# Optimization experiments

Measured on AMD Instinct MI355X. Metric: run time of the kernel, lower is better.

The kernel has to match this reference:

```python
import jax, jax.numpy as jnp
import numpy as np

NUM_HEADS = 12
HEAD_DIM = 64
HIDDEN = NUM_HEADS * HEAD_DIM  # 768


def setup_inputs() -> dict:
    key = jax.random.key(0)
    ks = jax.random.split(key, 18)
    B, Ni, Nt, H = 8, 1024, 512, HIDDEN
    inp = {
        "hidden_states": jax.random.normal(ks[0], (B, Ni, H), jnp.float32),
        "text": jax.random.normal(ks[1], (B, Nt, H), jnp.float32),
    }
    names = ["Wq", "Wk", "Wv", "Wqt", "Wkt", "Wvt", "Wo"]
    for i, n in enumerate(names):
        inp[n] = jax.random.normal(ks[2 + i], (H, H), jnp.float32) * 0.02
        inp["b" + n[1:]] = jnp.zeros((H,), jnp.float32)
    return inp


def _split_heads(x):
    # [B, S, H] -> [B, h, S, dh]
    B, S, _ = x.shape
    return x.reshape(B, S, NUM_HEADS, HEAD_DIM).transpose(0, 2, 1, 3)


def _merge_heads(x):
    # [B, h, S, dh] -> [B, S, H]
    B, h, S, dh = x.shape
    return x.transpose(0, 2, 1, 3).reshape(B, S, h * dh)


def _attend(q, k, v):
    scale = 1.0 / jnp.sqrt(jnp.asarray(HEAD_DIM, q.dtype))
    scores = jnp.einsum("bhqd,bhkd->bhqk", q, k) * scale
    probs = jax.nn.softmax(scores, axis=-1)
    ctx = jnp.einsum("bhqk,bhkd->bhqd", probs, v)
    return ctx, probs


def reference(hidden_states, text, Wq, bq, Wk, bk, Wv, bv,
              Wqt, bqt, Wkt, bkt, Wvt, bvt, Wo, bo):
    q_i = _split_heads(hidden_states @ Wq + bq)
    k_i = _split_heads(hidden_states @ Wk + bk)
    v_i = _split_heads(hidden_states @ Wv + bv)
    q_t = _split_heads(text @ Wqt + bqt)
    k_t = _split_heads(text @ Wkt + bkt)
    v_t = _split_heads(text @ Wvt + bvt)

    ctx_ii, weights = _attend(q_i, k_i, v_i)   # img -> img (weights returned, vis=True)
    ctx_tt, _ = _attend(q_t, k_t, v_t)         # text -> text
    ctx_it, _ = _attend(q_i, k_t, v_t)         # img queries, text keys/values
    ctx_ti, _ = _attend(q_t, k_i, v_i)         # text queries, img keys/values

    out_img = (_merge_heads(ctx_ii) + _merge_heads(ctx_it)) * 0.5 @ Wo + bo
    out_text = (_merge_heads(ctx_tt) + _merge_heads(ctx_ti)) * 0.5 @ Wo + bo
    return out_img, out_text, weights
```

## Files before the change

### kernel.cpp

```cpp
#include <hip/hip_runtime.h>

typedef __attribute__((ext_vector_type(4))) float f32x4;
typedef __attribute__((ext_vector_type(8))) short short8;
typedef __attribute__((ext_vector_type(4))) unsigned short us4;
typedef unsigned short u16;

__device__ __forceinline__ u16 f2b(float f) {
  union { float f; unsigned u; } a; a.f = f;
  unsigned r = a.u + 0x7fffu + ((a.u >> 16) & 1u);
  return (u16)(r >> 16);
}
#define SWZ(r, byteoff) ((((r) * 128) + (byteoff)) ^ (((r) & 7) << 4))

typedef __attribute__((address_space(1))) const void* gp1;
typedef __attribute__((address_space(3))) void* lp3;
__device__ __forceinline__ void gload16(const void* g, void* lds_wave_uniform_base) {
  __builtin_amdgcn_global_load_lds((gp1)g, (lp3)lds_wave_uniform_base, 16, 0, 0);
}

__global__ __launch_bounds__(256) void wtrans_kernel(
    const float* w0, const float* w1, const float* w2, const float* w3,
    const float* w4, const float* w5, const float* w6, u16* wt)
{
  const float* Ws[7] = {w0, w1, w2, w3, w4, w5, w6};
  const float* W = Ws[blockIdx.z];
  u16* out = wt + (size_t)blockIdx.z * 768 * 768;
  __shared__ float tile[64][65];
  const int t = threadIdx.x;
  const int r0 = blockIdx.y * 64, c0 = blockIdx.x * 64;
#pragma unroll
  for (int i = 0; i < 4; ++i) {
    int idx = i * 256 + t;
    int r = idx >> 4, c = (idx & 15) * 4;
    f32x4 v = *(const f32x4*)(W + (size_t)(r0 + r) * 768 + (c0 + c));
    tile[r][c + 0] = v[0]; tile[r][c + 1] = v[1];
    tile[r][c + 2] = v[2]; tile[r][c + 3] = v[3];
  }
  __syncthreads();
#pragma unroll
  for (int i = 0; i < 4; ++i) {
    int idx = i * 256 + t;
    int rn = idx >> 4, c = (idx & 15) * 4;
    us4 o;
    o[0] = f2b(tile[c + 0][rn]); o[1] = f2b(tile[c + 1][rn]);
    o[2] = f2b(tile[c + 2][rn]); o[3] = f2b(tile[c + 3][rn]);
    *(us4*)(out + (size_t)(c0 + rn) * 768 + (r0 + c)) = o;
  }
}

__global__ __launch_bounds__(256) void xconv_kernel(
    const float* __restrict__ h, const float* __restrict__ tx, u16* __restrict__ o)
{
  size_t e = ((size_t)blockIdx.x * 256 + threadIdx.x) * 8;
  const float* src; size_t off;
  if (e < 6291456) { src = h; off = e; } else { src = tx; off = e - 6291456; }
  f32x4 v0 = *(const f32x4*)(src + off), v1 = *(const f32x4*)(src + off + 4);
  short8 r;
  r[0] = (short)f2b(v0[0]); r[1] = (short)f2b(v0[1]); r[2] = (short)f2b(v0[2]); r[3] = (short)f2b(v0[3]);
  r[4] = (short)f2b(v1[0]); r[5] = (short)f2b(v1[1]); r[6] = (short)f2b(v1[2]); r[7] = (short)f2b(v1[3]);
  *(short8*)(o + e) = r;
}

__global__ __launch_bounds__(256) void proj_kernel(
    const u16* __restrict__ Xb, const u16* __restrict__ Wt3,
    const float* __restrict__ ba, const float* __restrict__ bb, const float* __restrict__ bc,
    u16* __restrict__ oa, u16* __restrict__ ob, u16* __restrict__ oc,
    int S, int logS)
{
  const int m0 = blockIdx.x * 128;
  const int y = blockIdx.y;
  const int z = y / 6;
  const int n0 = (y % 6) * 128;
  const u16* Wt = Wt3 + (size_t)y * 128 * 768;
  const float* bias = (z == 0) ? ba : (z == 1) ? bb : bc;
  u16* out = (z == 0) ? oa : (z == 1) ? ob : oc;
  const bool vmode = (z == 2);
  __shared__ unsigned char sm[36864];
  unsigned char* Asm = sm;
  unsigned char* Bsm = sm + 16384;
  const int t = threadIdx.x, w = t >> 6, l = t & 63;
  const int wm = (w & 1) * 64, wn = (w >> 1) * 64;
  f32x4 acc[4][4] = {};
  for (int k0 = 0; k0 < 768; k0 += 64) {
#pragma unroll
    for (int j = 0; j < 4; ++j) {
      int chunk = j * 4 + w;
      int r = chunk * 8 + (l >> 3);
      int cb = ((l & 7) * 16) ^ ((r & 7) << 4);
      gload16(Xb + (size_t)(m0 + r) * 768 + k0 + cb / 2, Asm + chunk * 1024);
    }
#pragma unroll
    for (int j = 0; j < 4; ++j) {
      int chunk = j * 4 + w;
      int r = chunk * 8 + (l >> 3);
      int cb = ((l & 7) * 16) ^ ((r & 7) << 4);
      gload16(Wt + (size_t)r * 768 + k0 + cb / 2, Bsm + chunk * 1024);
    }
    __syncthreads();
#pragma unroll
    for (int kc = 0; kc < 2; ++kc) {
      short8 af[4], bfr[4];
      const int koff = (kc * 32 + (l >> 4) * 8) * 2;
#pragma unroll
      for (int ms = 0; ms < 4; ++ms) {
        int row = wm + ms * 16 + (l & 15);
        af[ms] = *(const short8*)(Asm + SWZ(row, koff));
      }
#pragma unroll
      for (int ns = 0; ns < 4; ++ns) {
        int row = wn + ns * 16 + (l & 15);
        bfr[ns] = *(const short8*)(Bsm + SWZ(row, koff));
      }
#pragma unroll
      for (int ms = 0; ms < 4; ++ms)
#pragma unroll
        for (int ns = 0; ns < 4; ++ns)
          acc[ms][ns] = __builtin_amdgcn_mfma_f32_16x16x32_bf16(af[ms], bfr[ns], acc[ms][ns], 0, 0, 0);
    }
    __syncthreads();
  }
  float bv[4];
#pragma unroll
  for (int ns = 0; ns < 4; ++ns) bv[ns] = bias[n0 + wn + ns * 16 + (l & 15)];
#pragma unroll
  for (int ms = 0; ms < 4; ++ms)
#pragma unroll
    for (int ns = 0; ns < 4; ++ns)
#pragma unroll
      for (int i = 0; i < 4; ++i) {
        u16 u = f2b(acc[ms][ns][i] + bv[ns]);
        int mm = wm + ms * 16 + (l >> 4) * 4 + i;
        int nn = wn + ns * 16 + (l & 15);
        int row = vmode ? nn : mm, col = vmode ? mm : nn;
        *(u16*)(sm + row * 272 + col * 2) = u;
      }
  __syncthreads();
  if (!vmode) {
#pragma unroll
    for (int i = 0; i < 8; ++i) {
      int idx = i * 256 + t;
      int r = idx >> 4, c = (idx & 15) * 8;
      short8 v = *(const short8*)(sm + r * 272 + c * 2);
      int sg = m0 + r, b = sg >> logS, s = sg & (S - 1);
      int n = n0 + c, hh = n >> 6, d = n & 63;
      *(short8*)(out + (((size_t)b * 12 + hh) * S + s) * 64 + d) = v;
    }
  } else {
#pragma unroll
    for (int i = 0; i < 8; ++i) {
      int idx = i * 256 + t;
      int r = idx >> 4, c = (idx & 15) * 8;
      short8 v = *(const short8*)(sm + r * 272 + c * 2);
      int n = n0 + r, hh = n >> 6, d = n & 63;
      int sg = m0 + c, b = sg >> logS, s = sg & (S - 1);
      *(short8*)(out + (((size_t)b * 12 + hh) * 64 + d) * S + s) = v;
    }
  }
}

__device__ __forceinline__ void stage_k(const u16* Kp, int kt, unsigned char* Ksm, int w, int l) {
#pragma unroll
  for (int j = 0; j < 2; ++j) {
    int chunk = j * 4 + w;
    int r = chunk * 8 + (l >> 3);
    int cb = ((l & 7) * 16) ^ ((r & 7) << 4);
    gload16(Kp + (size_t)(kt * 64 + r) * 64 + cb / 2, Ksm + chunk * 1024);
  }
}
__device__ __forceinline__ void stage_v(const u16* Vp, int kt, int Sk, unsigned char* Vsm, int w, int l) {
#pragma unroll
  for (int j = 0; j < 2; ++j) {
    int chunk = j * 4 + w;
    int r = chunk * 8 + (l >> 3);
    int cb = ((l & 7) * 16) ^ ((r & 7) << 4);
    gload16(Vp + (size_t)r * Sk + kt * 64 + cb / 2, Vsm + chunk * 1024);
  }
}
__device__ __forceinline__ void qk_mfma(const short8 qf[2], const unsigned char* Ksm, int l, f32x4 sfr[4]) {
#pragma unroll
  for (int kc = 0; kc < 2; ++kc)
#pragma unroll
    for (int sub = 0; sub < 4; ++sub) {
      int row = sub * 16 + (l & 15);
      short8 kf = *(const short8*)(Ksm + SWZ(row, (kc * 32 + (l >> 4) * 8) * 2));
      sfr[sub] = __builtin_amdgcn_mfma_f32_16x16x32_bf16(qf[kc], kf, sfr[sub], 0, 0, 0);
    }
}
__device__ __forceinline__ void red16(float v[4]) {
#pragma unroll
  for (int d = 1; d < 16; d <<= 1)
#pragma unroll
    for (int i = 0; i < 4; ++i) v[i] += __shfl_xor(v[i], d);
}
__device__ __forceinline__ void attn_unnorm_pass(
    const u16* Kp, const u16* Vp, int Sk, const short8 qf[2],
    unsigned char* Ksm, unsigned char* Vsm, unsigned char* Psm,
    int w, int l, f32x4 og[4], float ll[4])
{
  const int nkt = Sk >> 6;
  for (int kt = 0; kt < nkt; ++kt) {
    stage_k(Kp, kt, Ksm, w, l);
    stage_v(Vp, kt, Sk, Vsm, w, l);
    __syncthreads();
    f32x4 sfr[4] = {};
    qk_mfma(qf, Ksm, l, sfr);
#pragma unroll
    for (int sub = 0; sub < 4; ++sub)
#pragma unroll
      for (int i = 0; i < 4; ++i) {
        float p = __expf(sfr[sub][i] * 0.125f);
        ll[i] += p;
        *(u16*)(Psm + SWZ((l >> 4) * 4 + i, (sub * 16 + (l & 15)) * 2)) = f2b(p);
      }
    short8 pa[2];
    pa[0] = *(const short8*)(Psm + SWZ(l & 15, ((l >> 4) * 8) * 2));
    pa[1] = *(const short8*)(Psm + SWZ(l & 15, (32 + (l >> 4) * 8) * 2));
#pragma unroll
    for (int kc = 0; kc < 2; ++kc)
#pragma unroll
      for (int ds = 0; ds < 4; ++ds) {
        int row = ds * 16 + (l & 15);
        short8 vb = *(const short8*)(Vsm + SWZ(row, (kc * 32 + (l >> 4) * 8) * 2));
        og[ds] = __builtin_amdgcn_mfma_f32_16x16x32_bf16(pa[kc], vb, og[ds], 0, 0, 0);
      }
    __syncthreads();
  }
}

__global__ __launch_bounds__(256) void attn2_kernel(
    const u16* __restrict__ Q,
    const u16* __restrict__ KA, const u16* __restrict__ VA, int SkA,
    const u16* __restrict__ KB, const u16* __restrict__ VB, int SkB,
    u16* __restrict__ CTX, float* __restrict__ PROBS, int Sq)
{
  const int h = blockIdx.y, b = blockIdx.z;
  const int q0 = blockIdx.x * 64;
  const int t = threadIdx.x, w = t >> 6, l = t & 63;
  const size_t bh = (size_t)b * 12 + h;
  const u16* Qp = Q + bh * (size_t)Sq * 64;
  const u16* KpA = KA + bh * (size_t)SkA * 64;
  const u16* VpA = VA + bh * (size_t)64 * SkA;
  const u16* KpB = KB + bh * (size_t)SkB * 64;
  const u16* VpB = VB + bh * (size_t)64 * SkB;
  __shared__ unsigned char smem[41984];
  unsigned char* Ksm = smem;
  unsigned char* Vsm = smem + 8192;
  unsigned char* Psm = smem + 16384 + w * 2048;
  unsigned char* Pf  = smem + 24576 + w * 4352;

  short8 qf[2];
  {
    int row = q0 + w * 16 + (l & 15);
    qf[0] = *(const short8*)(Qp + (size_t)row * 64 + (l >> 4) * 8);
    qf[1] = *(const short8*)(Qp + (size_t)row * 64 + 32 + (l >> 4) * 8);
  }

  f32x4 of[4] = {};
  if (PROBS) {
    float ll[4] = {0.f, 0.f, 0.f, 0.f};
    const int nkt = SkA >> 6;
    for (int kt = 0; kt < nkt; ++kt) {
      stage_k(KpA, kt, Ksm, w, l);
      __syncthreads();
      f32x4 sfr[4] = {};
      qk_mfma(qf, Ksm, l, sfr);
#pragma unroll
      for (int sub = 0; sub < 4; ++sub)
#pragma unroll
        for (int i = 0; i < 4; ++i) ll[i] += __expf(sfr[sub][i] * 0.125f);
      __syncthreads();
    }
    red16(ll);
    float rl[4];
#pragma unroll
    for (int i = 0; i < 4; ++i) rl[i] = 1.0f / ll[i];
    const size_t pbase = (bh * Sq + q0 + w * 16);
    for (int kt = 0; kt < nkt; ++kt) {
      stage_k(KpA, kt, Ksm, w, l);
      stage_v(VpA, kt, SkA, Vsm, w, l);
      __syncthreads();
      f32x4 sfr[4] = {};
      qk_mfma(qf, Ksm, l, sfr);
#pragma unroll
      for (int sub = 0; sub < 4; ++sub)
#pragma unroll
        for (int i = 0; i < 4; ++i) {
          float p = __expf(sfr[sub][i] * 0.125f) * rl[i];
          int prow = (l >> 4) * 4 + i, pcol = sub * 16 + (l & 15);
          *(float*)(Pf + prow * 272 + pcol * 4) = p;
          *(u16*)(Psm + SWZ(prow, pcol * 2)) = f2b(p);
        }
#pragma unroll
      for (int ps = 0; ps < 4; ++ps) {
        int row = ps * 4 + (l >> 4);
        f32x4 v = *(const f32x4*)(Pf + row * 272 + (l & 15) * 16);
        *(f32x4*)(PROBS + (pbase + row) * (size_t)SkA + kt * 64 + (l & 15) * 4) = v;
      }
      short8 pa[2];
      pa[0] = *(const short8*)(Psm + SWZ(l & 15, ((l >> 4) * 8) * 2));
      pa[1] = *(const short8*)(Psm + SWZ(l & 15, (32 + (l >> 4) * 8) * 2));
#pragma unroll
      for (int kc = 0; kc < 2; ++kc)
#pragma unroll
        for (int ds = 0; ds < 4; ++ds) {
          int row = ds * 16 + (l & 15);
          short8 vb = *(const short8*)(Vsm + SWZ(row, (kc * 32 + (l >> 4) * 8) * 2));
          of[ds] = __builtin_amdgcn_mfma_f32_16x16x32_bf16(pa[kc], vb, of[ds], 0, 0, 0);
        }
      __syncthreads();
    }
#pragma unroll
    for (int ds = 0; ds < 4; ++ds) of[ds] *= 0.5f;
  } else {
    float ll[4] = {0.f, 0.f, 0.f, 0.f};
    attn_unnorm_pass(KpA, VpA, SkA, qf, Ksm, Vsm, Psm, w, l, of, ll);
    red16(ll);
#pragma unroll
    for (int ds = 0; ds < 4; ++ds)
#pragma unroll
      for (int i = 0; i < 4; ++i) of[ds][i] *= 0.5f / ll[i];
  }
  {
    f32x4 og[4] = {};
    float l2[4] = {0.f, 0.f, 0.f, 0.f};
    attn_unnorm_pass(KpB, VpB, SkB, qf, Ksm, Vsm, Psm, w, l, og, l2);
    red16(l2);
#pragma unroll
    for (int ds = 0; ds < 4; ++ds)
#pragma unroll
      for (int i = 0; i < 4; ++i) of[ds][i] += og[ds][i] * (0.5f / l2[i]);
  }
#pragma unroll
  for (int ds = 0; ds < 4; ++ds)
#pragma unroll
    for (int i = 0; i < 4; ++i) {
      int prow = (l >> 4) * 4 + i, pcol = ds * 16 + (l & 15);
      *(u16*)(Psm + SWZ(prow, pcol * 2)) = f2b(of[ds][i]);
    }
#pragma unroll
  for (int i = 0; i < 2; ++i) {
    int idx = i * 64 + l;
    int r = idx >> 3, off = (idx & 7) * 16;
    short8 v = *(const short8*)(Psm + SWZ(r, off));
    int s = q0 + w * 16 + r;
    *(short8*)(CTX + ((size_t)b * Sq + s) * 768 + h * 64 + off / 2) = v;
  }
}

__global__ __launch_bounds__(256) void outproj_kernel(
    const u16* __restrict__ C, const u16* __restrict__ Wt,
    const float* __restrict__ bias, float* __restrict__ OUT)
{
  const int m0 = blockIdx.x * 128, n0 = blockIdx.y * 128;
  __shared__ unsigned char sm[32768];
  unsigned char* Asm = sm;
  unsigned char* Bsm = sm + 16384;
  const int t = threadIdx.x, w = t >> 6, l = t & 63;
  const int wm = (w & 1) * 64, wn = (w >> 1) * 64;
  f32x4 acc[4][4] = {};
  for (int k0 = 0; k0 < 768; k0 += 64) {
#pragma unroll
    for (int j = 0; j < 4; ++j) {
      int chunk = j * 4 + w;
      int r = chunk * 8 + (l >> 3);
      int cb = ((l & 7) * 16) ^ ((r & 7) << 4);
      gload16(C + (size_t)(m0 + r) * 768 + k0 + cb / 2, Asm + chunk * 1024);
    }
#pragma unroll
    for (int j = 0; j < 4; ++j) {
      int chunk = j * 4 + w;
      int r = chunk * 8 + (l >> 3);
      int cb = ((l & 7) * 16) ^ ((r & 7) << 4);
      gload16(Wt + (size_t)(n0 + r) * 768 + k0 + cb / 2, Bsm + chunk * 1024);
    }
    __syncthreads();
#pragma unroll
    for (int kc = 0; kc < 2; ++kc) {
      short8 af[4], bfr[4];
      const int koff = (kc * 32 + (l >> 4) * 8) * 2;
#pragma unroll
      for (int ms = 0; ms < 4; ++ms) {
        int row = wm + ms * 16 + (l & 15);
        af[ms] = *(const short8*)(Asm + SWZ(row, koff));
      }
#pragma unroll
      for (int ns = 0; ns < 4; ++ns) {
        int row = wn + ns * 16 + (l & 15);
        bfr[ns] = *(const short8*)(Bsm + SWZ(row, koff));
      }
#pragma unroll
      for (int ms = 0; ms < 4; ++ms)
#pragma unroll
        for (int ns = 0; ns < 4; ++ns)
          acc[ms][ns] = __builtin_amdgcn_mfma_f32_16x16x32_bf16(af[ms], bfr[ns], acc[ms][ns], 0, 0, 0);
    }
    __syncthreads();
  }
#pragma unroll
  for (int ms = 0; ms < 4; ++ms)
#pragma unroll
    for (int ns = 0; ns < 4; ++ns) {
      float bv = bias[n0 + wn + ns * 16 + (l & 15)];
#pragma unroll
      for (int i = 0; i < 4; ++i) {
        int mm = m0 + wm + ms * 16 + (l >> 4) * 4 + i;
        int nn = n0 + wn + ns * 16 + (l & 15);
        OUT[(size_t)mm * 768 + nn] = acc[ms][ns][i] + bv;
      }
    }
}

extern "C" void kernel_launch(void* const* d_in, const int* in_sizes, int n_in,
                              void* d_out, int out_size, void* d_ws, size_t ws_size,
                              hipStream_t stream)
{
  const float* hidden = (const float*)d_in[0];
  const float* text   = (const float*)d_in[1];
  const float* Wq  = (const float*)d_in[2];  const float* bq  = (const float*)d_in[3];
  const float* Wk  = (const float*)d_in[4];  const float* bk  = (const float*)d_in[5];
  const float* Wv  = (const float*)d_in[6];  const float* bv  = (const float*)d_in[7];
  const float* Wqt = (const float*)d_in[8];  const float* bqt = (const float*)d_in[9];
  const float* Wkt = (const float*)d_in[10]; const float* bkt = (const float*)d_in[11];
  const float* Wvt = (const float*)d_in[12]; const float* bvt = (const float*)d_in[13];
  const float* Wo  = (const float*)d_in[14]; const float* bo  = (const float*)d_in[15];

  u16* wt   = (u16*)d_ws;
  u16* xb   = wt + 7 * 589824;
  u16* qi   = xb + 9437184;
  u16* ki   = qi + 6291456;
  u16* vti  = ki + 6291456;
  u16* qt   = vti + 6291456;
  u16* ktx  = qt + 3145728;
  u16* vtt  = ktx + 3145728;
  u16* cimg = vtt + 3145728;
  u16* ctxt = cimg + 6291456;

  float* out_img  = (float*)d_out;
  float* out_text = out_img + 6291456;
  float* weights  = out_text + 3145728;

  wtrans_kernel<<<dim3(12, 12, 7), 256, 0, stream>>>(Wq, Wk, Wv, Wqt, Wkt, Wvt, Wo, wt);
  xconv_kernel<<<4608, 256, 0, stream>>>(hidden, text, xb);

  u16* wto = wt + 6 * 589824;
  proj_kernel<<<dim3(64, 18), 256, 0, stream>>>(xb, wt, bq, bk, bv, qi, ki, vti, 1024, 10);
  proj_kernel<<<dim3(32, 18), 256, 0, stream>>>(xb + 6291456, wt + 3 * 589824,
                                                bqt, bkt, bvt, qt, ktx, vtt, 512, 9);

  attn2_kernel<<<dim3(16, 12, 8), 256, 0, stream>>>(qi, ki, vti, 1024, ktx, vtt, 512,
                                                    cimg, weights, 1024);
  attn2_kernel<<<dim3(8, 12, 8), 256, 0, stream>>>(qt, ktx, vtt, 512, ki, vti, 1024,
                                                   ctxt, nullptr, 512);

  outproj_kernel<<<dim3(64, 6), 256, 0, stream>>>(cimg, wto, bo, out_img);
  outproj_kernel<<<dim3(32, 6), 256, 0, stream>>>(ctxt, wto, bo, out_text);
}
```

Baseline: 363.4 us.

## Merge launches, double-buffer K/V in attention, add MFMA priority hints

Merges the weight-transpose and input-conversion kernels into one launch, and merges the image and text variants of the projection, attention and output-projection kernels into single launches. Each merged kernel uses a remapped block index so work is spread across the XCDs. The attention kernel double-buffers the K/V tiles in LDS so the next tile loads while the current one is computed, which removes one barrier per iteration. It also keeps probabilities in fp32 LDS and converts them to bf16 right before the PV MFMA. s_setprio hints are wrapped around the MFMA loops, and LDS use per attention block grows, which may lower occupancy.

```diff
diff --git a/kernel.cpp b/kernel.cpp
--- a/kernel.cpp
+++ b/kernel.cpp
@@ -4,6 +4,7 @@
 typedef __attribute__((ext_vector_type(8))) short short8;
 typedef __attribute__((ext_vector_type(4))) unsigned short us4;
 typedef unsigned short u16;
+typedef unsigned char uchar;
 
 __device__ __forceinline__ u16 f2b(float f) {
   union { float f; unsigned u; } a; a.f = f;
@@ -18,62 +19,70 @@
   __builtin_amdgcn_global_load_lds((gp1)g, (lp3)lds_wave_uniform_base, 16, 0, 0);
 }
 
-__global__ __launch_bounds__(256) void wtrans_kernel(
+__global__ __launch_bounds__(256) void prep_kernel(
     const float* w0, const float* w1, const float* w2, const float* w3,
-    const float* w4, const float* w5, const float* w6, u16* wt)
+    const float* w4, const float* w5, const float* w6, u16* wt,
+    const float* __restrict__ h, const float* __restrict__ tx, u16* __restrict__ xb)
 {
-  const float* Ws[7] = {w0, w1, w2, w3, w4, w5, w6};
-  const float* W = Ws[blockIdx.z];
-  u16* out = wt + (size_t)blockIdx.z * 768 * 768;
-  __shared__ float tile[64][65];
-  const int t = threadIdx.x;
-  const int r0 = blockIdx.y * 64, c0 = blockIdx.x * 64;
-#pragma unroll
-  for (int i = 0; i < 4; ++i) {
-    int idx = i * 256 + t;
-    int r = idx >> 4, c = (idx & 15) * 4;
-    f32x4 v = *(const f32x4*)(W + (size_t)(r0 + r) * 768 + (c0 + c));
-    tile[r][c + 0] = v[0]; tile[r][c + 1] = v[1];
-    tile[r][c + 2] = v[2]; tile[r][c + 3] = v[3];
-  }
-  __syncthreads();
-#pragma unroll
-  for (int i = 0; i < 4; ++i) {
-    int idx = i * 256 + t;
-    int rn = idx >> 4, c = (idx & 15) * 4;
-    us4 o;
-    o[0] = f2b(tile[c + 0][rn]); o[1] = f2b(tile[c + 1][rn]);
-    o[2] = f2b(tile[c + 2][rn]); o[3] = f2b(tile[c + 3][rn]);
-    *(us4*)(out + (size_t)(c0 + rn) * 768 + (r0 + c)) = o;
-  }
-}
-
-__global__ __launch_bounds__(256) void xconv_kernel(
-    const float* __restrict__ h, const float* __restrict__ tx, u16* __restrict__ o)
+  const int bid = blockIdx.x, t = threadIdx.x;
+  if (bid < 1008) {
+    __shared__ float tile[64][65];
+    const float* Ws[7] = {w0, w1, w2, w3, w4, w5, w6};
+    int z = bid / 144, rem = bid % 144;
+    const float* W = Ws[z];
+    u16* out = wt + (size_t)z * 589824;
+    const int r0 = (rem / 12) * 64, c0 = (rem % 12) * 64;
+#pragma unroll
+    for (int i = 0; i < 4; ++i) {
+      int idx = i * 256 + t;
+      int r = idx >> 4, c = (idx & 15) * 4;
+      f32x4 v = *(const f32x4*)(W + (size_t)(r0 + r) * 768 + (c0 + c));
+      tile[r][c + 0] = v[0]; tile[r][c + 1] = v[1];
+      tile[r][c + 2] = v[2]; tile[r][c + 3] = v[3];
+    }
+    __syncthreads();
+#pragma unroll
+    for (int i = 0; i < 4; ++i) {
+      int idx = i * 256 + t;
+      int rn = idx >> 4, c = (idx & 15) * 4;
+      us4 o;
+      o[0] = f2b(tile[c + 0][rn]); o[1] = f2b(tile[c + 1][rn]);
+      o[2] = f2b(tile[c + 2][rn]); o[3] = f2b(tile[c + 3][rn]);
+      *(us4*)(out + (size_t)(c0 + rn) * 768 + (r0 + c)) = o;
+    }
+  } else {
+    size_t e = ((size_t)(bid - 1008) * 256 + t) * 8;
+    const float* src; size_t off;
+    if (e < 6291456) { src = h; off = e; } else { src = tx; off = e - 6291456; }
+    f32x4 v0 = *(const f32x4*)(src + off), v1 = *(const f32x4*)(src + off + 4);
+    short8 r;
+    r[0] = (short)f2b(v0[0]); r[1] = (short)f2b(v0[1]); r[2] = (short)f2b(v0[2]); r[3] = (short)f2b(v0[3]);
+    r[4] = (short)f2b(v1[0]); r[5] = (short)f2b(v1[1]); r[6] = (short)f2b(v1[2]); r[7] = (short)f2b(v1[3]);
+    *(short8*)(xb + e) = r;
+  }
+}
+
+__global__ __launch_bounds__(256) void proj_kernel(
+    const u16* __restrict__ Xb, const u16* __restrict__ wt,
+    const float* __restrict__ bq, const float* __restrict__ bk, const float* __restrict__ bv,
+    const float* __restrict__ bqt, const float* __restrict__ bkt, const float* __restrict__ bvt,
+    u16* __restrict__ qi, u16* __restrict__ ki, u16* __restrict__ vti,
+    u16* __restrict__ qt, u16* __restrict__ ktx, u16* __restrict__ vtt)
 {
-  size_t e = ((size_t)blockIdx.x * 256 + threadIdx.x) * 8;
-  const float* src; size_t off;
-  if (e < 6291456) { src = h; off = e; } else { src = tx; off = e - 6291456; }
-  f32x4 v0 = *(const f32x4*)(src + off), v1 = *(const f32x4*)(src + off + 4);
-  short8 r;
-  r[0] = (short)f2b(v0[0]); r[1] = (short)f2b(v0[1]); r[2] = (short)f2b(v0[2]); r[3] = (short)f2b(v0[3]);
-  r[4] = (short)f2b(v1[0]); r[5] = (short)f2b(v1[1]); r[6] = (short)f2b(v1[2]); r[7] = (short)f2b(v1[3]);
-  *(short8*)(o + e) = r;
-}
-
-__global__ __launch_bounds__(256) void proj_kernel(
-    const u16* __restrict__ Xb, const u16* __restrict__ Wt3,
-    const float* __restrict__ ba, const float* __restrict__ bb, const float* __restrict__ bc,
-    u16* __restrict__ oa, u16* __restrict__ ob, u16* __restrict__ oc,
-    int S, int logS)
-{
-  const int m0 = blockIdx.x * 128;
-  const int y = blockIdx.y;
-  const int z = y / 6;
-  const int n0 = (y % 6) * 128;
-  const u16* Wt = Wt3 + (size_t)y * 128 * 768;
-  const float* bias = (z == 0) ? ba : (z == 1) ? bb : bc;
-  u16* out = (z == 0) ? oa : (z == 1) ? ob : oc;
+  const int bid = blockIdx.x;
+  const int wk = (bid & 7) * 216 + (bid >> 3);
+  const bool img = wk < 1152;
+  const int id = img ? wk : wk - 1152;
+  const int y = img ? (id >> 6) : (id >> 5);
+  const int x = img ? (id & 63) : (id & 31);
+  const int z = y / 6, n0 = (y % 6) * 128, m0 = x * 128;
+  const int S = img ? 1024 : 512, logS = img ? 10 : 9;
+  const u16* X = img ? Xb : Xb + 6291456;
+  const u16* Wt = wt + (img ? 0 : (size_t)3 * 589824) + (size_t)y * 98304;
+  const float* bias = img ? (z == 0 ? bq : z == 1 ? bk : bv)
+                          : (z == 0 ? bqt : z == 1 ? bkt : bvt);
+  u16* out = img ? (z == 0 ? qi : z == 1 ? ki : vti)
+                 : (z == 0 ? qt : z == 1 ? ktx : vtt);
   const bool vmode = (z == 2);
   __shared__ unsigned char sm[36864];
   unsigned char* Asm = sm;
@@ -87,7 +96,7 @@
       int chunk = j * 4 + w;
       int r = chunk * 8 + (l >> 3);
       int cb = ((l & 7) * 16) ^ ((r & 7) << 4);
-      gload16(Xb + (size_t)(m0 + r) * 768 + k0 + cb / 2, Asm + chunk * 1024);
+      gload16(X + (size_t)(m0 + r) * 768 + k0 + cb / 2, Asm + chunk * 1024);
     }
 #pragma unroll
     for (int j = 0; j < 4; ++j) {
@@ -111,24 +120,26 @@
         int row = wn + ns * 16 + (l & 15);
         bfr[ns] = *(const short8*)(Bsm + SWZ(row, koff));
       }
+      __builtin_amdgcn_s_setprio(1);
 #pragma unroll
       for (int ms = 0; ms < 4; ++ms)
 #pragma unroll
         for (int ns = 0; ns < 4; ++ns)
           acc[ms][ns] = __builtin_amdgcn_mfma_f32_16x16x32_bf16(af[ms], bfr[ns], acc[ms][ns], 0, 0, 0);
-    }
-    __syncthreads();
-  }
-  float bv[4];
-#pragma unroll
-  for (int ns = 0; ns < 4; ++ns) bv[ns] = bias[n0 + wn + ns * 16 + (l & 15)];
+      __builtin_amdgcn_s_setprio(0);
+    }
+    __syncthreads();
+  }
+  float bvv[4];
+#pragma unroll
+  for (int ns = 0; ns < 4; ++ns) bvv[ns] = bias[n0 + wn + ns * 16 + (l & 15)];
 #pragma unroll
   for (int ms = 0; ms < 4; ++ms)
 #pragma unroll
     for (int ns = 0; ns < 4; ++ns)
 #pragma unroll
       for (int i = 0; i < 4; ++i) {
-        u16 u = f2b(acc[ms][ns][i] + bv[ns]);
+        u16 u = f2b(acc[ms][ns][i] + bvv[ns]);
         int mm = wm + ms * 16 + (l >> 4) * 4 + i;
         int nn = wn + ns * 16 + (l & 15);
         int row = vmode ? nn : mm, col = vmode ? mm : nn;
@@ -158,7 +169,7 @@
   }
 }
 
-__device__ __forceinline__ void stage_k(const u16* Kp, int kt, unsigned char* Ksm, int w, int l) {
+__device__ __forceinline__ void stage_k(const u16* Kp, int kt, uchar* Ksm, int w, int l) {
 #pragma unroll
   for (int j = 0; j < 2; ++j) {
     int chunk = j * 4 + w;
@@ -167,7 +178,7 @@
     gload16(Kp + (size_t)(kt * 64 + r) * 64 + cb / 2, Ksm + chunk * 1024);
   }
 }
-__device__ __forceinline__ void stage_v(const u16* Vp, int kt, int Sk, unsigned char* Vsm, int w, int l) {
+__device__ __forceinline__ void stage_v(const u16* Vp, int kt, int Sk, uchar* Vsm, int w, int l) {
 #pragma unroll
   for (int j = 0; j < 2; ++j) {
     int chunk = j * 4 + w;
@@ -176,7 +187,8 @@
     gload16(Vp + (size_t)r * Sk + kt * 64 + cb / 2, Vsm + chunk * 1024);
   }
 }
-__device__ __forceinline__ void qk_mfma(const short8 qf[2], const unsigned char* Ksm, int l, f32x4 sfr[4]) {
+__device__ __forceinline__ void qk8(const short8 qf[2], const uchar* Ksm, int l, f32x4 sfr[4]) {
+  __builtin_amdgcn_s_setprio(1);
 #pragma unroll
   for (int kc = 0; kc < 2; ++kc)
 #pragma unroll
@@ -185,6 +197,29 @@
       short8 kf = *(const short8*)(Ksm + SWZ(row, (kc * 32 + (l >> 4) * 8) * 2));
       sfr[sub] = __builtin_amdgcn_mfma_f32_16x16x32_bf16(qf[kc], kf, sfr[sub], 0, 0, 0);
     }
+  __builtin_amdgcn_s_setprio(0);
+}
+__device__ __forceinline__ void pv8(const uchar* Pf, const uchar* Vsm, int l, f32x4 og[4]) {
+  const uchar* base = Pf + (l & 15) * 272 + (l >> 4) * 32;
+  f32x4 a0 = *(const f32x4*)(base);
+  f32x4 a1 = *(const f32x4*)(base + 16);
+  f32x4 b0 = *(const f32x4*)(base + 128);
+  f32x4 b1 = *(const f32x4*)(base + 144);
+  short8 pa0, pa1;
+  pa0[0] = (short)f2b(a0[0]); pa0[1] = (short)f2b(a0[1]); pa0[2] = (short)f2b(a0[2]); pa0[3] = (short)f2b(a0[3]);
+  pa0[4] = (short)f2b(a1[0]); pa0[5] = (short)f2b(a1[1]); pa0[6] = (short)f2b(a1[2]); pa0[7] = (short)f2b(a1[3]);
+  pa1[0] = (short)f2b(b0[0]); pa1[1] = (short)f2b(b0[1]); pa1[2] = (short)f2b(b0[2]); pa1[3] = (short)f2b(b0[3]);
+  pa1[4] = (short)f2b(b1[0]); pa1[5] = (short)f2b(b1[1]); pa1[6] = (short)f2b(b1[2]); pa1[7] = (short)f2b(b1[3]);
+  __builtin_amdgcn_s_setprio(1);
+#pragma unroll
+  for (int ds = 0; ds < 4; ++ds) {
+    int row = ds * 16 + (l & 15);
+    short8 vb0 = *(const short8*)(Vsm + SWZ(row, ((l >> 4) * 8) * 2));
+    short8 vb1 = *(const short8*)(Vsm + SWZ(row, (32 + (l >> 4) * 8) * 2));
+    og[ds] = __builtin_amdgcn_mfma_f32_16x16x32_bf16(pa0, vb0, og[ds], 0, 0, 0);
+    og[ds] = __builtin_amdgcn_mfma_f32_16x16x32_bf16(pa1, vb1, og[ds], 0, 0, 0);
+  }
+  __builtin_amdgcn_s_setprio(0);
 }
 __device__ __forceinline__ void red16(float v[4]) {
 #pragma unroll
@@ -192,61 +227,67 @@
 #pragma unroll
     for (int i = 0; i < 4; ++i) v[i] += __shfl_xor(v[i], d);
 }
-__device__ __forceinline__ void attn_unnorm_pass(
+__device__ __forceinline__ void pass_unnorm(
     const u16* Kp, const u16* Vp, int Sk, const short8 qf[2],
-    unsigned char* Ksm, unsigned char* Vsm, unsigned char* Psm,
+    uchar* Ks0, uchar* Ks1, uchar* Vs0, uchar* Vs1, uchar* Pf,
     int w, int l, f32x4 og[4], float ll[4])
 {
   const int nkt = Sk >> 6;
+  stage_k(Kp, 0, Ks0, w, l);
+  stage_v(Vp, 0, Sk, Vs0, w, l);
+  __syncthreads();
   for (int kt = 0; kt < nkt; ++kt) {
-    stage_k(Kp, kt, Ksm, w, l);
-    stage_v(Vp, kt, Sk, Vsm, w, l);
-    __syncthreads();
+    uchar* Kc = (kt & 1) ? Ks1 : Ks0;
+    uchar* Vc = (kt & 1) ? Vs1 : Vs0;
+    if (kt + 1 < nkt) {
+      stage_k(Kp, kt + 1, (kt & 1) ? Ks0 : Ks1, w, l);
+      stage_v(Vp, kt + 1, Sk, (kt & 1) ? Vs0 : Vs1, w, l);
+    }
     f32x4 sfr[4] = {};
-    qk_mfma(qf, Ksm, l, sfr);
+    qk8(qf, Kc, l, sfr);
 #pragma unroll
     for (int sub = 0; sub < 4; ++sub)
 #pragma unroll
       for (int i = 0; i < 4; ++i) {
         float p = __expf(sfr[sub][i] * 0.125f);
         ll[i] += p;
-        *(u16*)(Psm + SWZ((l >> 4) * 4 + i, (sub * 16 + (l & 15)) * 2)) = f2b(p);
-      }
-    short8 pa[2];
-    pa[0] = *(const short8*)(Psm + SWZ(l & 15, ((l >> 4) * 8) * 2));
-    pa[1] = *(const short8*)(Psm + SWZ(l & 15, (32 + (l >> 4) * 8) * 2));
-#pragma unroll
-    for (int kc = 0; kc < 2; ++kc)
-#pragma unroll
-      for (int ds = 0; ds < 4; ++ds) {
-        int row = ds * 16 + (l & 15);
-        short8 vb = *(const short8*)(Vsm + SWZ(row, (kc * 32 + (l >> 4) * 8) * 2));
-        og[ds] = __builtin_amdgcn_mfma_f32_16x16x32_bf16(pa[kc], vb, og[ds], 0, 0, 0);
-      }
-    __syncthreads();
-  }
-}
-
-__global__ __launch_bounds__(256) void attn2_kernel(
-    const u16* __restrict__ Q,
-    const u16* __restrict__ KA, const u16* __restrict__ VA, int SkA,
-    const u16* __restrict__ KB, const u16* __restrict__ VB, int SkB,
-    u16* __restrict__ CTX, float* __restrict__ PROBS, int Sq)
+        *(float*)(Pf + ((l >> 4) * 4 + i) * 272 + (sub * 16 + (l & 15)) * 4) = p;
+      }
+    pv8(Pf, Vc, l, og);
+    __syncthreads();
+  }
+}
+
+__global__ __launch_bounds__(256) void attn_kernel(
+    const u16* __restrict__ qi, const u16* __restrict__ ki, const u16* __restrict__ vti,
+    const u16* __restrict__ qt, const u16* __restrict__ ktx, const u16* __restrict__ vtt,
+    u16* __restrict__ cimg, u16* __restrict__ ctxt, float* __restrict__ weights)
 {
-  const int h = blockIdx.y, b = blockIdx.z;
-  const int q0 = blockIdx.x * 64;
+  __shared__ uchar smem[50176];
   const int t = threadIdx.x, w = t >> 6, l = t & 63;
-  const size_t bh = (size_t)b * 12 + h;
-  const u16* Qp = Q + bh * (size_t)Sq * 64;
-  const u16* KpA = KA + bh * (size_t)SkA * 64;
-  const u16* VpA = VA + bh * (size_t)64 * SkA;
-  const u16* KpB = KB + bh * (size_t)SkB * 64;
-  const u16* VpB = VB + bh * (size_t)64 * SkB;
-  __shared__ unsigned char smem[41984];
-  unsigned char* Ksm = smem;
-  unsigned char* Vsm = smem + 8192;
-  unsigned char* Psm = smem + 16384 + w * 2048;
-  unsigned char* Pf  = smem + 24576 + w * 4352;
+  uchar* Ks0 = smem;
+  uchar* Ks1 = smem + 8192;
+  uchar* Vs0 = smem + 16384;
+  uchar* Vs1 = smem + 24576;
+  uchar* Pf  = smem + 32768 + w * 4352;
+
+  const int bid = blockIdx.x;
+  const int wk = (bid & 7) * 288 + (bid >> 3);
+  const bool img = wk < 1536;
+  const int id = img ? wk : wk - 1536;
+  const int x = img ? (id & 15) : (id & 7);
+  const int head = img ? (id >> 4) : (id >> 3);
+  const int b = head / 12, h = head % 12;
+  const int Sq = img ? 1024 : 512;
+  const int SkA = img ? 1024 : 512, SkB = img ? 512 : 1024;
+  const u16* Qp = (img ? qi : qt) + (size_t)head * Sq * 64;
+  const u16* KpA = (img ? ki : ktx) + (size_t)head * SkA * 64;
+  const u16* VpA = (img ? vti : vtt) + (size_t)head * 64 * SkA;
+  const u16* KpB = (img ? ktx : ki) + (size_t)head * SkB * 64;
+  const u16* VpB = (img ? vtt : vti) + (size_t)head * 64 * SkB;
+  u16* CTX = img ? cimg : ctxt;
+  float* PROBS = img ? weights : nullptr;
+  const int q0 = x * 64;
 
   short8 qf[2];
   {
@@ -259,36 +300,42 @@
   if (PROBS) {
     float ll[4] = {0.f, 0.f, 0.f, 0.f};
     const int nkt = SkA >> 6;
+    stage_k(KpA, 0, Ks0, w, l);
+    __syncthreads();
     for (int kt = 0; kt < nkt; ++kt) {
-      stage_k(KpA, kt, Ksm, w, l);
-      __syncthreads();
+      uchar* Kc = (kt & 1) ? Ks1 : Ks0;
+      if (kt + 1 < nkt) stage_k(KpA, kt + 1, (kt & 1) ? Ks0 : Ks1, w, l);
       f32x4 sfr[4] = {};
-      qk_mfma(qf, Ksm, l, sfr);
+      qk8(qf, Kc, l, sfr);
 #pragma unroll
       for (int sub = 0; sub < 4; ++sub)
 #pragma unroll
         for (int i = 0; i < 4; ++i) ll[i] += __expf(sfr[sub][i] * 0.125f);
       __syncthreads();
     }
+    stage_k(KpA, 0, Ks0, w, l);
+    stage_v(VpA, 0, SkA, Vs0, w, l);
     red16(ll);
     float rl[4];
 #pragma unroll
     for (int i = 0; i < 4; ++i) rl[i] = 1.0f / ll[i];
-    const size_t pbase = (bh * Sq + q0 + w * 16);
+    __syncthreads();
+    const size_t pbase = ((size_t)head * Sq + q0 + w * 16);
     for (int kt = 0; kt < nkt; ++kt) {
-      stage_k(KpA, kt, Ksm, w, l);
-      stage_v(VpA, kt, SkA, Vsm, w, l);
-      __syncthreads();
+      uchar* Kc = (kt & 1) ? Ks1 : Ks0;
+      uchar* Vc = (kt & 1) ? Vs1 : Vs0;
+      if (kt + 1 < nkt) {
+        stage_k(KpA, kt + 1, (kt & 1) ? Ks0 : Ks1, w, l);
+        stage_v(VpA, kt + 1, SkA, (kt & 1) ? Vs0 : Vs1, w, l);
+      }
       f32x4 sfr[4] = {};
-      qk_mfma(qf, Ksm, l, sfr);
+      qk8(qf, Kc, l, sfr);
 #pragma unroll
       for (int sub = 0; sub < 4; ++sub)
 #pragma unroll
         for (int i = 0; i < 4; ++i) {
           float p = __expf(sfr[sub][i] * 0.125f) * rl[i];
-          int prow = (l >> 4) * 4 + i, pcol = sub * 16 + (l & 15);
-          *(float*)(Pf + prow * 272 + pcol * 4) = p;
-          *(u16*)(Psm + SWZ(prow, pcol * 2)) = f2b(p);
+          *(float*)(Pf + ((l >> 4) * 4 + i) * 272 + (sub * 16 + (l & 15)) * 4) = p;
         }
 #pragma unroll
       for (int ps = 0; ps < 4; ++ps) {
@@ -296,24 +343,14 @@
         f32x4 v = *(const f32x4*)(Pf + row * 272 + (l & 15) * 16);
         *(f32x4*)(PROBS + (pbase + row) * (size_t)SkA + kt * 64 + (l & 15) * 4) = v;
       }
-      short8 pa[2];
-      pa[0] = *(const short8*)(Psm + SWZ(l & 15, ((l >> 4) * 8) * 2));
-      pa[1] = *(const short8*)(Psm + SWZ(l & 15, (32 + (l >> 4) * 8) * 2));
-#pragma unroll
-      for (int kc = 0; kc < 2; ++kc)
-#pragma unroll
-        for (int ds = 0; ds < 4; ++ds) {
-          int row = ds * 16 + (l & 15);
-          short8 vb = *(const short8*)(Vsm + SWZ(row, (kc * 32 + (l >> 4) * 8) * 2));
-          of[ds] = __builtin_amdgcn_mfma_f32_16x16x32_bf16(pa[kc], vb, of[ds], 0, 0, 0);
-        }
+      pv8(Pf, Vc, l, of);
       __syncthreads();
     }
 #pragma unroll
     for (int ds = 0; ds < 4; ++ds) of[ds] *= 0.5f;
   } else {
     float ll[4] = {0.f, 0.f, 0.f, 0.f};
-    attn_unnorm_pass(KpA, VpA, SkA, qf, Ksm, Vsm, Psm, w, l, of, ll);
+    pass_unnorm(KpA, VpA, SkA, qf, Ks0, Ks1, Vs0, Vs1, Pf, w, l, of, ll);
     red16(ll);
 #pragma unroll
     for (int ds = 0; ds < 4; ++ds)
@@ -323,7 +360,7 @@
   {
     f32x4 og[4] = {};
     float l2[4] = {0.f, 0.f, 0.f, 0.f};
-    attn_unnorm_pass(KpB, VpB, SkB, qf, Ksm, Vsm, Psm, w, l, og, l2);
+    pass_unnorm(KpB, VpB, SkB, qf, Ks0, Ks1, Vs0, Vs1, Pf, w, l, og, l2);
     red16(l2);
 #pragma unroll
     for (int ds = 0; ds < 4; ++ds)
@@ -333,25 +370,36 @@
 #pragma unroll
   for (int ds = 0; ds < 4; ++ds)
 #pragma unroll
-    for (int i = 0; i < 4; ++i) {
-      int prow = (l >> 4) * 4 + i, pcol = ds * 16 + (l & 15);
-      *(u16*)(Psm + SWZ(prow, pcol * 2)) = f2b(of[ds][i]);
-    }
+    for (int i = 0; i < 4; ++i)
+      *(float*)(Pf + ((l >> 4) * 4 + i) * 272 + (ds * 16 + (l & 15)) * 4) = of[ds][i];
 #pragma unroll
   for (int i = 0; i < 2; ++i) {
-    int idx = i * 64 + l;
-    int r = idx >> 3, off = (idx & 7) * 16;
-    short8 v = *(const short8*)(Psm + SWZ(r, off));
+    int it = i * 64 + l;
+    int r = it >> 3, cg = it & 7;
+    f32x4 v0 = *(const f32x4*)(Pf + r * 272 + cg * 32);
+    f32x4 v1 = *(const f32x4*)(Pf + r * 272 + cg * 32 + 16);
+    short8 o;
+    o[0] = (short)f2b(v0[0]); o[1] = (short)f2b(v0[1]); o[2] = (short)f2b(v0[2]); o[3] = (short)f2b(v0[3]);
+    o[4] = (short)f2b(v1[0]); o[5] = (short)f2b(v1[1]); o[6] = (short)f2b(v1[2]); o[7] = (short)f2b(v1[3]);
     int s = q0 + w * 16 + r;
-    *(short8*)(CTX + ((size_t)b * Sq + s) * 768 + h * 64 + off / 2) = v;
+    *(short8*)(CTX + ((size_t)b * Sq + s) * 768 + h * 64 + cg * 8) = o;
   }
 }
 
 __global__ __launch_bounds__(256) void outproj_kernel(
-    const u16* __restrict__ C, const u16* __restrict__ Wt,
-    const float* __restrict__ bias, float* __restrict__ OUT)
+    const u16* __restrict__ cimg, const u16* __restrict__ ctxt,
+    const u16* __restrict__ Wto, const float* __restrict__ bias,
+    float* __restrict__ out_img, float* __restrict__ out_text)
 {
-  const int m0 = blockIdx.x * 128, n0 = blockIdx.y * 128;
+  const int bid = blockIdx.x;
+  const int wk = (bid & 7) * 72 + (bid >> 3);
+  const bool img = wk < 384;
+  const int id = img ? wk : wk - 384;
+  const int y = img ? (id >> 6) : (id >> 5);
+  const int x = img ? (id & 63) : (id & 31);
+  const u16* C = img ? cimg : ctxt;
+  float* OUT = img ? out_img : out_text;
+  const int m0 = x * 128, n0 = y * 128;
   __shared__ unsigned char sm[32768];
   unsigned char* Asm = sm;
   unsigned char* Bsm = sm + 16384;
@@ -371,7 +419,7 @@
       int chunk = j * 4 + w;
       int r = chunk * 8 + (l >> 3);
       int cb = ((l & 7) * 16) ^ ((r & 7) << 4);
-      gload16(Wt + (size_t)(n0 + r) * 768 + k0 + cb / 2, Bsm + chunk * 1024);
+      gload16(Wto + (size_t)(n0 + r) * 768 + k0 + cb / 2, Bsm + chunk * 1024);
     }
     __syncthreads();
 #pragma unroll
@@ -388,11 +436,13 @@
         int row = wn + ns * 16 + (l & 15);
         bfr[ns] = *(const short8*)(Bsm + SWZ(row, koff));
       }
+      __builtin_amdgcn_s_setprio(1);
 #pragma unroll
       for (int ms = 0; ms < 4; ++ms)
 #pragma unroll
         for (int ns = 0; ns < 4; ++ns)
           acc[ms][ns] = __builtin_amdgcn_mfma_f32_16x16x32_bf16(af[ms], bfr[ns], acc[ms][ns], 0, 0, 0);
+      __builtin_amdgcn_s_setprio(0);
     }
     __syncthreads();
   }
@@ -439,19 +489,12 @@
   float* out_text = out_img + 6291456;
   float* weights  = out_text + 3145728;
 
-  wtrans_kernel<<<dim3(12, 12, 7), 256, 0, stream>>>(Wq, Wk, Wv, Wqt, Wkt, Wvt, Wo, wt);
-  xconv_kernel<<<4608, 256, 0, stream>>>(hidden, text, xb);
-
-  u16* wto = wt + 6 * 589824;
-  proj_kernel<<<dim3(64, 18), 256, 0, stream>>>(xb, wt, bq, bk, bv, qi, ki, vti, 1024, 10);
-  proj_kernel<<<dim3(32, 18), 256, 0, stream>>>(xb + 6291456, wt + 3 * 589824,
-                                                bqt, bkt, bvt, qt, ktx, vtt, 512, 9);
-
-  attn2_kernel<<<dim3(16, 12, 8), 256, 0, stream>>>(qi, ki, vti, 1024, ktx, vtt, 512,
-                                                    cimg, weights, 1024);
-  attn2_kernel<<<dim3(8, 12, 8), 256, 0, stream>>>(qt, ktx, vtt, 512, ki, vti, 1024,
-                                                   ctxt, nullptr, 512);
-
-  outproj_kernel<<<dim3(64, 6), 256, 0, stream>>>(cimg, wto, bo, out_img);
-  outproj_kernel<<<dim3(32, 6), 256, 0, stream>>>(ctxt, wto, bo, out_text);
-}
+  prep_kernel<<<5616, 256, 0, stream>>>(Wq, Wk, Wv, Wqt, Wkt, Wvt, Wo, wt,
+                                        hidden, text, xb);
+  proj_kernel<<<1728, 256, 0, stream>>>(xb, wt, bq, bk, bv, bqt, bkt, bvt,
+                                        qi, ki, vti, qt, ktx, vtt);
+  attn_kernel<<<2304, 256, 0, stream>>>(qi, ki, vti, qt, ktx, vtt,
+                                        cimg, ctxt, weights);
+  outproj_kernel<<<576, 256, 0, stream>>>(cimg, ctxt, wt + 6 * 589824, bo,
+                                          out_img, out_text);
+}
```

After: 319.7 us. 1.14x faster.
